# Kernel tuning notes

Measured on AMD Instinct MI355X. Metric: run time of the kernel, lower is better.

## Reference

```python
import jax, jax.numpy as jnp
import numpy as np

D = 768      # embedding_dim
M = 3072     # mlp_dim
G = 4        # num_expert_groups
E = 8        # experts_per_group
KG = 2       # k_groups
KE = 4       # k_experts
EPS = 1e-6   # gate weight threshold from the torch module


def setup_inputs() -> dict:
    key = jax.random.key(0)
    ks = jax.random.split(key, 9)
    x = jax.random.normal(ks[0], (1, 1024, D), dtype=jnp.float32)
    Wg = jax.random.normal(ks[1], (D, G), dtype=jnp.float32) * 0.02
    bg = jax.random.normal(ks[2], (G,), dtype=jnp.float32) * 0.01
    We = jax.random.normal(ks[3], (G, D, E), dtype=jnp.float32) * 0.02
    be = jax.random.normal(ks[4], (G, E), dtype=jnp.float32) * 0.01
    W1 = jax.random.normal(ks[5], (G, E, D, M), dtype=jnp.float32) * 0.02
    b1 = jax.random.normal(ks[6], (G, E, M), dtype=jnp.float32) * 0.01
    W2 = jax.random.normal(ks[7], (G, E, M, D), dtype=jnp.float32) * 0.02
    b2 = jax.random.normal(ks[8], (G, E, D), dtype=jnp.float32) * 0.01
    return {"x": x, "Wg": Wg, "bg": bg, "We": We, "be": be,
            "W1": W1, "b1": b1, "W2": W2, "b2": b2}


def _topk_gates(logits, k):
    # top-k logits -> softmax over the k entries, then zero out weights < 1e-6
    top, idx = jax.lax.top_k(logits, k)
    gates = jax.nn.softmax(top, axis=-1)
    gates = jnp.where(gates >= EPS, gates, jnp.zeros_like(gates))
    return gates, idx


def reference(x, Wg, bg, We, be, W1, b1, W2, b2):
    orig_shape = x.shape
    xf = x.reshape(-1, D)  # [N, D]

    # ---- level 1: group gating (eval mode: clean logits, no noise) ----
    glog = xf @ Wg + bg                      # [N, G]
    ggates, gidx = _topk_gates(glog, KG)     # [N, KG]
    gw = jnp.einsum('nk,nkg->ng', ggates,
                    jax.nn.one_hot(gidx, G, dtype=xf.dtype))  # dense [N, G]

    # ---- level 2: expert gating within each group ----
    # computed densely for all groups; unselected groups get zero group weight
    elog = jnp.einsum('nd,gde->nge', xf, We) + be  # [N, G, E]
    egates, eidx = _topk_gates(elog, KE)            # [N, G, KE]
    ew = jnp.einsum('ngk,ngke->nge', egates,
                    jax.nn.one_hot(eidx, E, dtype=xf.dtype))  # dense [N, G, E]

    combine = gw[:, :, None] * ew  # [N, G, E] combine weights

    # ---- expert MLPs (dense compute, combine-weighted sum) ----
    y = jnp.zeros_like(xf)
    for g in range(G):  # small fixed loop over expert groups
        h = jax.nn.gelu(jnp.einsum('nd,edm->enm', xf, W1[g]) + b1[g][:, None, :],
                        approximate=False)               # [E, N, M]
        o = jnp.einsum('enm,emd->end', h, W2[g]) + b2[g][:, None, :]  # [E, N, D]
        y = y + jnp.einsum('end,ne->nd', o, combine[:, g, :])
    return y.reshape(orig_shape)
```

## Files before the change

kernel.cpp:

```cpp
#include <hip/hip_runtime.h>
#include <hip/hip_bf16.h>
#include <math.h>

#define NTOK 1024
#define DDIM 768
#define MDIM 3072
#define GN 4
#define EN 8
#define NEXP 32
#define NPAIR 8192
#define EPSW 1e-6f
#define BYSPAN 3

typedef __attribute__((ext_vector_type(4))) float f32x4;
typedef __attribute__((ext_vector_type(4))) int   i32x4;
typedef __attribute__((ext_vector_type(4))) unsigned short u16x4;
typedef __attribute__((ext_vector_type(8))) __bf16 bf16x8;

__device__ __forceinline__ unsigned short f2bf(float f) {
  unsigned u = __builtin_bit_cast(unsigned, f);
  u += 0x7FFFu + ((u >> 16) & 1u);
  return (unsigned short)(u >> 16);
}

__global__ void init_kernel(int* __restrict__ p) { p[threadIdx.x] = 0; }

__global__ __launch_bounds__(256) void zero_y(float* __restrict__ y) {
  ((f32x4*)y)[blockIdx.x * 256 + threadIdx.x] = (f32x4){0.f, 0.f, 0.f, 0.f};
}

__global__ __launch_bounds__(256) void x2bf(const float* __restrict__ x,
                                            unsigned short* __restrict__ xb) {
  const int i = (blockIdx.x * 256 + threadIdx.x) * 16;
#pragma unroll
  for (int j = 0; j < 4; ++j) {
    const f32x4 v = *(const f32x4*)(x + i + j * 4);
    u16x4 p = { f2bf(v.x), f2bf(v.y), f2bf(v.z), f2bf(v.w) };
    *(u16x4*)(xb + i + j * 4) = p;
  }
}

__global__ __launch_bounds__(256) void gating_kernel(
    const float* __restrict__ x, const float* __restrict__ Wg,
    const float* __restrict__ bg, const float* __restrict__ We,
    const float* __restrict__ be, int* __restrict__ counts,
    int* __restrict__ pair_e, float* __restrict__ pair_w)
{
  __shared__ float xr[DDIM];
  __shared__ float logits[36];
  const int n = blockIdx.x;
  const int tid = threadIdx.x;
  const float* xp = x + (size_t)n * DDIM;
  for (int d = tid; d < DDIM; d += 256) xr[d] = xp[d];
  __syncthreads();

  const int w = tid >> 6, lane = tid & 63;
  for (int j = 0; j < 9; ++j) {
    const int o = w + 4 * j;
    float s = 0.f;
    if (o < 4) {
      for (int d = lane; d < DDIM; d += 64) s += xr[d] * Wg[d * GN + o];
    } else {
      const int g = (o - 4) >> 3, e = (o - 4) & 7;
      const float* wp = We + (size_t)g * DDIM * EN + e;
      for (int d = lane; d < DDIM; d += 64) s += xr[d] * wp[d * EN];
    }
    for (int off = 32; off; off >>= 1) s += __shfl_xor(s, off);
    if (lane == 0) logits[o] = s + ((o < 4) ? bg[o] : be[o - 4]);
  }
  __syncthreads();

  if (tid == 0) {
    float gl[4];
    for (int i = 0; i < 4; ++i) gl[i] = logits[i];
    int i0 = 0;
    for (int i = 1; i < 4; ++i) if (gl[i] > gl[i0]) i0 = i;
    int i1 = -1;
    for (int i = 0; i < 4; ++i) {
      if (i == i0) continue;
      if (i1 < 0 || gl[i] > gl[i1]) i1 = i;
    }
    const float m = gl[i0];
    const float e1 = expf(gl[i1] - m);
    const float s2 = 1.f + e1;
    float gv[2] = { 1.f / s2, e1 / s2 };
    int gi[2] = { i0, i1 };
    for (int r = 0; r < 2; ++r) if (gv[r] < EPSW) gv[r] = 0.f;

    for (int r = 0; r < 2; ++r) {
      const int g = gi[r];
      float el[8];
      for (int e = 0; e < 8; ++e) el[e] = logits[4 + g * 8 + e];
      int sel[4];
      for (int q = 0; q < 4; ++q) {
        int best = -1;
        for (int e = 0; e < 8; ++e) {
          bool used = false;
          for (int p = 0; p < q; ++p) if (sel[p] == e) used = true;
          if (used) continue;
          if (best < 0 || el[e] > el[best]) best = e;
        }
        sel[q] = best;
      }
      const float mm = el[sel[0]];
      float ex[4]; float ss = 0.f;
      for (int q = 0; q < 4; ++q) { ex[q] = expf(el[sel[q]] - mm); ss += ex[q]; }
      for (int q = 0; q < 4; ++q) {
        float ew = ex[q] / ss;
        if (ew < EPSW) ew = 0.f;
        const int gbl = g * 8 + sel[q];
        const int j = r * 4 + q;
        pair_e[n * 8 + j] = gbl;
        pair_w[n * 8 + j] = gv[r] * ew;
        atomicAdd(&counts[gbl], 1);
      }
    }
  }
}

__global__ void scan_kernel(const int* __restrict__ counts, int* __restrict__ offsets)
{
  if (threadIdx.x == 0) {
    int a = 0;
    for (int i = 0; i < NEXP; ++i) { offsets[i] = a; a += counts[i]; }
  }
}

__global__ __launch_bounds__(256) void scatter_kernel(
    const int* __restrict__ pair_e, const float* __restrict__ pair_w,
    const int* __restrict__ offsets, int* __restrict__ cursor,
    int* __restrict__ slot_tok, float* __restrict__ slot_w)
{
  const int idx = blockIdx.x * 256 + threadIdx.x;
  if (idx < NPAIR) {
    const int e = pair_e[idx];
    const int s = offsets[e] + atomicAdd(&cursor[e], 1);
    slot_tok[s] = idx >> 3;
    slot_w[s] = pair_w[idx];
  }
}

template<int K, int NLD, int EPI, int GATHER>
__global__ __launch_bounds__(256, 2) void moe_gemm_rs(
    const unsigned short* __restrict__ Abase, const float* __restrict__ W,
    const float* __restrict__ bias, const int* __restrict__ counts,
    const int* __restrict__ offsets, const float* __restrict__ slot_w,
    const int* __restrict__ slot_tok, unsigned short* __restrict__ Hout,
    float* __restrict__ Yout)
{
  constexpr int NT = K / 32;
  constexpr int BUFB = 16384;

  const int ge = blockIdx.z;
  const int cnt = counts[ge];
  const int nb = blockIdx.y;
  const int off = offsets[ge];
  const int tid = threadIdx.x;

  __shared__ __align__(16) unsigned char lds[2 * BUFB];

  const int am = tid >> 2, ac = tid & 3;
  const int asw0 = am * 64 + ((ac ^ ((am ^ (am >> 2)) & 3)) * 16);
  const int asw1 = asw0 + 4096;

  const int kq = tid >> 5, ln = tid & 31;
  const float* bp = W + (size_t)ge * K * NLD + (size_t)(kq * 4) * NLD + nb * 128 + ln;
  int bwr[4];
#pragma unroll
  for (int ii = 0; ii < 4; ++ii) {
    const int n = ln + 32 * ii;
    const int s = (n ^ (n >> 2)) & 3;
    bwr[ii] = 8192 + n * 64 + (((kq >> 1) ^ s) * 16) + ((kq & 1) * 8);
  }

  const int w = tid >> 6, lane = tid & 63;
  const int wr = (w >> 1) * 64, wc = (w & 1) * 64;
  const int l15 = lane & 15, l4 = lane >> 4;
  int aoff[4], boff[4];
#pragma unroll
  for (int mf = 0; mf < 4; ++mf) {
    const int m = wr + mf * 16 + l15;
    aoff[mf] = m * 64 + ((l4 ^ ((m ^ (m >> 2)) & 3)) * 16);
  }
#pragma unroll
  for (int nf = 0; nf < 4; ++nf) {
    const int n = wc + nf * 16 + l15;
    boff[nf] = 8192 + n * 64 + ((l4 ^ ((n ^ (n >> 2)) & 3)) * 16);
  }

  for (int by = blockIdx.x; by * 128 < cnt; by += BYSPAN) {
    int gr0 = by * 128 + am;      if (gr0 >= cnt) gr0 = cnt - 1;
    int gr1 = by * 128 + am + 64; if (gr1 >= cnt) gr1 = cnt - 1;
    const unsigned short* ap0;
    const unsigned short* ap1;
    if (GATHER) {
      ap0 = Abase + (size_t)slot_tok[off + gr0] * K + ac * 8;
      ap1 = Abase + (size_t)slot_tok[off + gr1] * K + ac * 8;
    } else {
      ap0 = Abase + (size_t)(off + gr0) * K + ac * 8;
      ap1 = Abase + (size_t)(off + gr1) * K + ac * 8;
    }

    f32x4 acc[4][4];
#pragma unroll
    for (int mf = 0; mf < 4; ++mf)
#pragma unroll
      for (int nf = 0; nf < 4; ++nf)
        acc[mf][nf] = (f32x4){0.f, 0.f, 0.f, 0.f};

    i32x4 aA0, aA1, aB0, aB1;
    float bA[16], bB[16];

#define LOADA(T, R0, R1) { \
    R0 = *(const i32x4*)(ap0 + (T) * 32); \
    R1 = *(const i32x4*)(ap1 + (T) * 32); }
#define LOADB(T, BS) { _Pragma("unroll") \
    for (int ii = 0; ii < 4; ++ii) { _Pragma("unroll") \
      for (int jj = 0; jj < 4; ++jj) \
        BS[ii * 4 + jj] = bp[(size_t)((T) * 32 + jj) * NLD + 32 * ii]; } }
#define CVTW(R0, R1, BS, BASE) { \
    *(i32x4*)((BASE) + asw0) = R0; \
    *(i32x4*)((BASE) + asw1) = R1; \
    _Pragma("unroll") \
    for (int ii = 0; ii < 4; ++ii) { \
      u16x4 p = { f2bf(BS[ii*4+0]), f2bf(BS[ii*4+1]), f2bf(BS[ii*4+2]), f2bf(BS[ii*4+3]) }; \
      *(u16x4*)((BASE) + bwr[ii]) = p; } }
#define COMPUTE(BASE) { bf16x8 afr[4], bfr[4]; _Pragma("unroll") \
    for (int mf = 0; mf < 4; ++mf) \
      afr[mf] = __builtin_bit_cast(bf16x8, *(const i32x4*)((BASE) + aoff[mf])); \
    _Pragma("unroll") \
    for (int nf = 0; nf < 4; ++nf) \
      bfr[nf] = __builtin_bit_cast(bf16x8, *(const i32x4*)((BASE) + boff[nf])); \
    _Pragma("unroll") \
    for (int mf = 0; mf < 4; ++mf) { _Pragma("unroll") \
      for (int nf = 0; nf < 4; ++nf) \
        acc[mf][nf] = __builtin_amdgcn_mfma_f32_16x16x32_bf16( \
            afr[mf], bfr[nf], acc[mf][nf], 0, 0, 0); } }

    LOADA(0, aA0, aA1); LOADB(0, bA);
    LOADA(1, aB0, aB1); LOADB(1, bB);

    for (int t = 0; t < NT; t += 2) {
      CVTW(aA0, aA1, bA, lds);
      if (t + 2 < NT) { LOADA(t + 2, aA0, aA1); LOADB(t + 2, bA); }
      asm volatile("s_waitcnt lgkmcnt(0)" ::: "memory");
      __builtin_amdgcn_s_barrier();
      COMPUTE(lds);
      asm volatile("" ::: "memory");
      __builtin_amdgcn_s_barrier();
      CVTW(aB0, aB1, bB, lds + BUFB);
      if (t + 3 < NT) { LOADA(t + 3, aB0, aB1); LOADB(t + 3, bB); }
      asm volatile("s_waitcnt lgkmcnt(0)" ::: "memory");
      __builtin_amdgcn_s_barrier();
      COMPUTE(lds + BUFB);
      asm volatile("" ::: "memory");
      __builtin_amdgcn_s_barrier();
    }
#undef LOADA
#undef LOADB
#undef CVTW
#undef COMPUTE

#pragma unroll
    for (int mf = 0; mf < 4; ++mf) {
      const int rb = by * 128 + wr + mf * 16 + l4 * 4;
      if constexpr (EPI == 0) {
#pragma unroll
        for (int nf = 0; nf < 4; ++nf) {
          const int col = nb * 128 + wc + nf * 16 + l15;
          const float bv = bias[(size_t)ge * NLD + col];
#pragma unroll
          for (int j = 0; j < 4; ++j) {
            const int r = rb + j;
            if (r < cnt) {
              const float v = acc[mf][nf][j] + bv;
              const float gl = 0.5f * v * (1.f + erff(v * 0.70710678118654752f));
              Hout[(size_t)(off + r) * NLD + col] = f2bf(gl);
            }
          }
        }
      } else {
#pragma unroll
        for (int j = 0; j < 4; ++j) {
          const int r = rb + j;
          if (r < cnt) {
            const int slot = off + r;
            const float sw = slot_w[slot];
            const int tok = slot_tok[slot];
#pragma unroll
            for (int nf = 0; nf < 4; ++nf) {
              const int col = nb * 128 + wc + nf * 16 + l15;
              const float v = acc[mf][nf][j] + bias[(size_t)ge * NLD + col];
              atomicAdd(&Yout[(size_t)tok * DDIM + col], sw * v);
            }
          }
        }
      }
    }
  }
}

extern "C" void kernel_launch(void* const* d_in, const int* in_sizes, int n_in,
                              void* d_out, int out_size, void* d_ws, size_t ws_size,
                              hipStream_t stream)
{
  const float* x  = (const float*)d_in[0];
  const float* Wg = (const float*)d_in[1];
  const float* bg = (const float*)d_in[2];
  const float* We = (const float*)d_in[3];
  const float* be = (const float*)d_in[4];
  const float* W1 = (const float*)d_in[5];
  const float* b1 = (const float*)d_in[6];
  const float* W2 = (const float*)d_in[7];
  const float* b2 = (const float*)d_in[8];
  float* y = (float*)d_out;

  char* ws = (char*)d_ws;
  int*   counts   = (int*)(ws + 0);
  int*   offsets  = (int*)(ws + 256);
  int*   cursor   = (int*)(ws + 512);
  int*   pair_e   = (int*)(ws + 1024);
  float* pair_w   = (float*)(ws + 33792);
  int*   slot_tok = (int*)(ws + 66560);
  float* slot_w   = (float*)(ws + 99328);
  unsigned short* xb = (unsigned short*)(ws + 132096);
  unsigned short* H  = (unsigned short*)(ws + 12715008);

  init_kernel<<<1, 256, 0, stream>>>((int*)ws);
  zero_y<<<NTOK * DDIM / 1024, 256, 0, stream>>>(y);
  x2bf<<<NTOK * DDIM / 4096, 256, 0, stream>>>(x, xb);
  gating_kernel<<<NTOK, 256, 0, stream>>>(x, Wg, bg, We, be, counts, pair_e, pair_w);
  scan_kernel<<<1, 64, 0, stream>>>(counts, offsets);
  scatter_kernel<<<NPAIR / 256, 256, 0, stream>>>(pair_e, pair_w, offsets, cursor,
                                                  slot_tok, slot_w);

  moe_gemm_rs<DDIM, MDIM, 0, 1><<<dim3(BYSPAN, MDIM / 128, NEXP), 256, 0, stream>>>(
      xb, W1, b1, counts, offsets, nullptr, slot_tok, H, nullptr);
  moe_gemm_rs<MDIM, DDIM, 1, 0><<<dim3(BYSPAN, DDIM / 128, NEXP), 256, 0, stream>>>(
      H, W2, b2, counts, offsets, slot_w, slot_tok, nullptr, y);
}
```

Baseline: 511.6 us.

## Triple-buffer register prefetch and drop the trailing barrier in GEMM main loop

The GEMM main loop now rotates three register sets for the A/B tile prefetch instead of two, unrolled by six. Global loads for tile t+2 are issued before the current tile is converted and written to LDS, which gives each load more time in flight. The second barrier per step is removed. The LDS double buffer stays safe because the barrier in the next step already orders every wave's reads of a buffer before it is rewritten. The cost is more registers and a requirement that the tile count be divisible by six, which holds for K=768 and K=3072.

```diff
diff --git a/kernel.cpp b/kernel.cpp
--- a/kernel.cpp
+++ b/kernel.cpp
@@ -208,8 +208,8 @@
       for (int nf = 0; nf < 4; ++nf)
         acc[mf][nf] = (f32x4){0.f, 0.f, 0.f, 0.f};
 
-    i32x4 aA0, aA1, aB0, aB1;
-    float bA[16], bB[16];
+    i32x4 aA0, aA1, aB0, aB1, aC0, aC1;
+    float bA[16], bB[16], bC[16];
 
 #define LOADA(T, R0, R1) { \
     R0 = *(const i32x4*)(ap0 + (T) * 32); \
@@ -236,30 +236,30 @@
       for (int nf = 0; nf < 4; ++nf) \
         acc[mf][nf] = __builtin_amdgcn_mfma_f32_16x16x32_bf16( \
             afr[mf], bfr[nf], acc[mf][nf], 0, 0, 0); } }
+#define STEP(T, C0, C1, CB, I0, I1, IB, BASE) { \
+    if ((T) + 2 < NT) { LOADA((T) + 2, I0, I1); LOADB((T) + 2, IB); } \
+    CVTW(C0, C1, CB, BASE); \
+    asm volatile("s_waitcnt lgkmcnt(0)" ::: "memory"); \
+    __builtin_amdgcn_s_barrier(); \
+    COMPUTE(BASE); \
+  }
 
     LOADA(0, aA0, aA1); LOADB(0, bA);
     LOADA(1, aB0, aB1); LOADB(1, bB);
 
-    for (int t = 0; t < NT; t += 2) {
-      CVTW(aA0, aA1, bA, lds);
-      if (t + 2 < NT) { LOADA(t + 2, aA0, aA1); LOADB(t + 2, bA); }
-      asm volatile("s_waitcnt lgkmcnt(0)" ::: "memory");
-      __builtin_amdgcn_s_barrier();
-      COMPUTE(lds);
-      asm volatile("" ::: "memory");
-      __builtin_amdgcn_s_barrier();
-      CVTW(aB0, aB1, bB, lds + BUFB);
-      if (t + 3 < NT) { LOADA(t + 3, aB0, aB1); LOADB(t + 3, bB); }
-      asm volatile("s_waitcnt lgkmcnt(0)" ::: "memory");
-      __builtin_amdgcn_s_barrier();
-      COMPUTE(lds + BUFB);
-      asm volatile("" ::: "memory");
-      __builtin_amdgcn_s_barrier();
+    for (int t = 0; t < NT; t += 6) {
+      STEP(t + 0, aA0, aA1, bA, aC0, aC1, bC, lds);
+      STEP(t + 1, aB0, aB1, bB, aA0, aA1, bA, lds + BUFB);
+      STEP(t + 2, aC0, aC1, bC, aB0, aB1, bB, lds);
+      STEP(t + 3, aA0, aA1, bA, aC0, aC1, bC, lds + BUFB);
+      STEP(t + 4, aB0, aB1, bB, aA0, aA1, bA, lds);
+      STEP(t + 5, aC0, aC1, bC, aB0, aB1, bB, lds + BUFB);
     }
 #undef LOADA
 #undef LOADB
 #undef CVTW
 #undef COMPUTE
+#undef STEP
 
 #pragma unroll
     for (int mf = 0; mf < 4; ++mf) {
```

Result: faster. 493.8 us (-3.5%).
